# Optimization experiments

Hardware: AMD Instinct MI355X
Metric: run time of the kernel (lower is better)

## Reference

```python
import jax, jax.numpy as jnp
import numpy as np

N_SAMPLES = 4096
BACKBONE_OUT = 512
EXPANSION = 8192
NUM_CLASSES = 1000
C_COEF = 1.0


def setup_inputs() -> dict:
    key = jax.random.key(0)
    k1, k2, k3, k4 = jax.random.split(key, 4)
    X = jax.random.normal(k1, (N_SAMPLES, BACKBONE_OUT), dtype=jnp.float32)
    W_buffer = jax.random.normal(k2, (BACKBONE_OUT, EXPANSION), dtype=jnp.float32) / np.sqrt(BACKBONE_OUT)
    W_main = jax.random.normal(k3, (EXPANSION, NUM_CLASSES), dtype=jnp.float32) / np.sqrt(EXPANSION)
    W_comp = jax.random.normal(k4, (EXPANSION, NUM_CLASSES), dtype=jnp.float32) / np.sqrt(EXPANSION)
    return {"X": X, "W_buffer": W_buffer, "W_main": W_main, "W_comp": W_comp, "k": 500}


def _knn_mean_cosine(Xe, k):
    # Xe: [N, D]. Cosine kNN (excluding self), then mean of neighbor features.
    N = Xe.shape[0]
    Xn = Xe / jnp.linalg.norm(Xe, axis=1, keepdims=True)
    sim = Xn @ Xn.T                                      # [N, N]
    diag = jnp.arange(N)
    sim = sim.at[diag, diag].set(-jnp.inf)               # exclude self (== indices[:,1:])
    _, idx = jax.lax.top_k(sim, k)                       # [N, k] nearest by cosine
    # Gather-mean via binary adjacency matmul (avoids [N,k,D] intermediate).
    rows = jnp.repeat(diag, k)
    A = jnp.zeros((N, N), Xe.dtype).at[rows, idx.reshape(-1)].set(1.0)
    return (A @ Xe) / jnp.asarray(k, Xe.dtype)           # [N, D]


def reference(X, W_buffer, W_main, W_comp, k):
    Xe = X @ W_buffer                                    # random buffer expansion [N, D]
    X_main = jnp.maximum(Xe, 0.0) @ W_main               # relu -> main analytic linear
    X_knn = _knn_mean_cosine(Xe, k)
    X_comp = jnp.tanh(X_knn) @ W_comp                    # tanh -> compensation linear
    return X_main + C_COEF * X_comp
```

## Files before the change

kernel.cpp:

```cpp
#include <hip/hip_runtime.h>
#include <hip/hip_bf16.h>

#define MSAMP 4096
#define D0    512
#define EXPN  8192
#define NCLS  1000
#define NPAD  1024
#define QSCALE     (6.0f / 127.0f)
#define QSCALE_INV (127.0f / 6.0f)

typedef __attribute__((ext_vector_type(8))) _Float16       half8;
typedef __attribute__((ext_vector_type(8))) unsigned short ushort8v;
typedef __attribute__((ext_vector_type(4))) float          f32x4;
typedef __attribute__((ext_vector_type(4))) int            i32x4v;

__device__ __forceinline__ unsigned short f2h(float f) {
    union { _Float16 h; unsigned short u; } c; c.h = (_Float16)f; return c.u;
}
__device__ __forceinline__ float h2f(unsigned short u) {
    union { unsigned short u; _Float16 h; } c; c.u = u; return (float)c.h;
}
__device__ __forceinline__ ushort8v relu8h(ushort8v v) {
#pragma unroll
    for (int j = 0; j < 8; ++j) v[j] = (v[j] & 0x8000u) ? (unsigned short)0 : v[j];
    return v;
}
__device__ __forceinline__ half8 as_half8(const unsigned short* p) {
    return *(const half8*)p;
}
__device__ __forceinline__ float tanh_fast(float x) {
    float e = __expf(2.0f * x);
    return 1.0f - 2.0f * __builtin_amdgcn_rcpf(e + 1.0f);
}

__global__ __launch_bounds__(256) void cvt_x(const float* __restrict__ src,
                                             unsigned short* __restrict__ dst)
{
    const size_t i = ((size_t)blockIdx.x * 256 + threadIdx.x) * 8;
    float4 v0 = *(const float4*)(src + i), v1 = *(const float4*)(src + i + 4);
    union { unsigned short u[8]; ushort8v v; } H;
    H.u[0] = f2h(v0.x); H.u[1] = f2h(v0.y); H.u[2] = f2h(v0.z); H.u[3] = f2h(v0.w);
    H.u[4] = f2h(v1.x); H.u[5] = f2h(v1.y); H.u[6] = f2h(v1.z); H.u[7] = f2h(v1.w);
    *(ushort8v*)(dst + i) = H.v;
}

__global__ void transpose_wb(const float* __restrict__ src,
                             unsigned short* __restrict__ dst)
{
    __shared__ float t[32][33];
    const int n0 = blockIdx.x * 32, k0 = blockIdx.y * 32;
    const int tx = threadIdx.x, ty = threadIdx.y;
#pragma unroll
    for (int i = 0; i < 4; ++i)
        t[ty + 8 * i][tx] = src[(size_t)(k0 + ty + 8 * i) * EXPN + n0 + tx];
    __syncthreads();
#pragma unroll
    for (int i = 0; i < 4; ++i)
        dst[(size_t)(n0 + ty + 8 * i) * D0 + k0 + tx] = f2h(t[tx][ty + 8 * i]);
}

__global__ __launch_bounds__(256) void gemm_xe_mfma(
    const unsigned short* __restrict__ Xh, const unsigned short* __restrict__ WbT,
    unsigned short* __restrict__ Xe)
{
    __shared__ __align__(16) char smem[34816];
    unsigned short (*AsF)[64][8] = (unsigned short (*)[64][8])(smem);
    unsigned short (*BsF)[64][8] = (unsigned short (*)[64][8])(smem + 8192);

    const int tid = threadIdx.x;
    const int wid = tid >> 6, lane = tid & 63;
    const int l15 = lane & 15, q = lane >> 4;
    const int wm = (wid >> 1) * 64, wn = (wid & 1) * 64;
    const int row0 = blockIdx.y * 128, col0 = blockIdx.x * 128;

    const int sr = tid >> 1;
    const int scp = (tid & 1) * 2;
    const int mi_w = sr >> 4, l_w = sr & 15;

    f32x4 acc[4][4];
#pragma unroll
    for (int m = 0; m < 4; ++m)
#pragma unroll
        for (int n = 0; n < 4; ++n) acc[m][n] = (f32x4){0.f, 0.f, 0.f, 0.f};

    for (int k0 = 0; k0 < D0; k0 += 32) {
        const unsigned short* pa = Xh  + (size_t)(row0 + sr) * D0 + k0 + scp * 8;
        const unsigned short* pb = WbT + (size_t)(col0 + sr) * D0 + k0 + scp * 8;
        ushort8v a0 = *(const ushort8v*)pa, a1 = *(const ushort8v*)(pa + 8);
        ushort8v b0 = *(const ushort8v*)pb, b1 = *(const ushort8v*)(pb + 8);

        __syncthreads();
        *(ushort8v*)&AsF[mi_w][scp * 16 + l_w][0] = a0;
        *(ushort8v*)&AsF[mi_w][(scp + 1) * 16 + l_w][0] = a1;
        *(ushort8v*)&BsF[mi_w][scp * 16 + l_w][0] = b0;
        *(ushort8v*)&BsF[mi_w][(scp + 1) * 16 + l_w][0] = b1;
        __syncthreads();

        half8 fa[4], fb[4];
#pragma unroll
        for (int m = 0; m < 4; ++m) {
            fa[m] = as_half8(&AsF[(wm >> 4) + m][lane][0]);
            fb[m] = as_half8(&BsF[(wn >> 4) + m][lane][0]);
        }
#pragma unroll
        for (int m = 0; m < 4; ++m)
#pragma unroll
            for (int n = 0; n < 4; ++n)
                acc[m][n] = __builtin_amdgcn_mfma_f32_16x16x32_f16(fa[m], fb[n], acc[m][n], 0, 0, 0);
    }

    unsigned short (*Cb)[136] = (unsigned short (*)[136])smem;
    const int rr = tid >> 1, hh = (tid & 1) * 64;
    __syncthreads();
#pragma unroll
    for (int m = 0; m < 4; ++m)
#pragma unroll
        for (int n = 0; n < 4; ++n)
#pragma unroll
            for (int r = 0; r < 4; ++r)
                Cb[wm + m * 16 + q * 4 + r][wn + n * 16 + l15] = f2h(acc[m][n][r]);
    __syncthreads();
#pragma unroll
    for (int c = 0; c < 8; ++c)
        *(ushort8v*)&Xe[(size_t)(row0 + rr) * EXPN + col0 + hh + c * 8] =
            *(const ushort8v*)&Cb[rr][hh + c * 8];
}

__global__ __launch_bounds__(256) void gemm_sim(
    const unsigned short* __restrict__ Xe,
    const float* __restrict__ invn, float* __restrict__ Sm)
{
    __shared__ unsigned short AsF[8][64][8], BsF[8][64][8];

    const int t = blockIdx.x;
    int bj = (int)((sqrtf(8.0f * t + 1.0f) - 1.0f) * 0.5f);
    while ((bj + 1) * (bj + 2) / 2 <= t) ++bj;
    while (bj * (bj + 1) / 2 > t) --bj;
    const int bi = t - bj * (bj + 1) / 2;
    const int row0 = bi * 128, col0 = bj * 128;

    const int tid = threadIdx.x;
    const int wid = tid >> 6, lane = tid & 63;
    const int l15 = lane & 15, q = lane >> 4;
    const int wm = (wid >> 1) * 64, wn = (wid & 1) * 64;

    const int sr = tid >> 1;
    const int scp = (tid & 1) * 2;
    const int mi_w = sr >> 4, l_w = sr & 15;

    f32x4 acc[4][4];
#pragma unroll
    for (int m = 0; m < 4; ++m)
#pragma unroll
        for (int n = 0; n < 4; ++n) acc[m][n] = (f32x4){0.f, 0.f, 0.f, 0.f};

    for (int k0 = 0; k0 < EXPN; k0 += 32) {
        const unsigned short* pa = Xe + (size_t)(row0 + sr) * EXPN + k0 + scp * 8;
        const unsigned short* pb = Xe + (size_t)(col0 + sr) * EXPN + k0 + scp * 8;
        ushort8v a0 = *(const ushort8v*)pa, a1 = *(const ushort8v*)(pa + 8);
        ushort8v b0 = *(const ushort8v*)pb, b1 = *(const ushort8v*)(pb + 8);

        __syncthreads();
        *(ushort8v*)&AsF[mi_w][scp * 16 + l_w][0] = a0;
        *(ushort8v*)&AsF[mi_w][(scp + 1) * 16 + l_w][0] = a1;
        *(ushort8v*)&BsF[mi_w][scp * 16 + l_w][0] = b0;
        *(ushort8v*)&BsF[mi_w][(scp + 1) * 16 + l_w][0] = b1;
        __syncthreads();

        half8 fa[4], fb[4];
#pragma unroll
        for (int m = 0; m < 4; ++m) {
            fa[m] = as_half8(&AsF[(wm >> 4) + m][lane][0]);
            fb[m] = as_half8(&BsF[(wn >> 4) + m][lane][0]);
        }
#pragma unroll
        for (int m = 0; m < 4; ++m)
#pragma unroll
            for (int n = 0; n < 4; ++n)
                acc[m][n] = __builtin_amdgcn_mfma_f32_16x16x32_f16(fa[m], fb[n], acc[m][n], 0, 0, 0);
    }

    const bool mirror = (bi != bj);
#pragma unroll
    for (int m = 0; m < 4; ++m)
#pragma unroll
        for (int n = 0; n < 4; ++n) {
            const int gj = col0 + wn + n * 16 + l15;
            const float invj = invn[gj];
#pragma unroll
            for (int r = 0; r < 4; ++r) {
                const int gi = row0 + wm + m * 16 + q * 4 + r;
                float v = acc[m][n][r] * invn[gi] * invj;
                if (gi == gj) v = -3.0e38f;
                Sm[(size_t)gi * MSAMP + gj] = v;
                if (mirror) Sm[(size_t)gj * MSAMP + gi] = v;
            }
        }
}

__global__ __launch_bounds__(256) void gemm_adj_i8(
    const unsigned* __restrict__ Abits, const signed char* __restrict__ XeT,
    unsigned short* __restrict__ Tk, const int* __restrict__ kp)
{
    __shared__ signed char BsF[8][64][16];
    __shared__ uint2 aw2[128];

    const int tid = threadIdx.x;
    const int wid = tid >> 6, lane = tid & 63;
    const int l15 = lane & 15, q = lane >> 4;
    const int wm = (wid >> 1) * 64, wn = (wid & 1) * 64;
    const int row0 = blockIdx.x * 128;
    const int col0 = blockIdx.y * 128;

    const int sr = tid >> 1;
    const int half = tid & 1;

    i32x4v acc[4][4];
#pragma unroll
    for (int m = 0; m < 4; ++m)
#pragma unroll
        for (int n = 0; n < 4; ++n) acc[m][n] = (i32x4v){0, 0, 0, 0};

    for (int k0 = 0; k0 < MSAMP; k0 += 64) {
        const signed char* pb = XeT + (size_t)(col0 + sr) * MSAMP + k0 + half * 32;
        i32x4v b0 = *(const i32x4v*)pb;
        i32x4v b1 = *(const i32x4v*)(pb + 16);
        uint2 wv = make_uint2(0u, 0u);
        if (tid < 128)
            wv = *(const uint2*)(Abits + (size_t)(row0 + tid) * (MSAMP / 32) + (k0 >> 5));

        __syncthreads();
        *(i32x4v*)&BsF[sr >> 4][(half * 2 + 0) * 16 + (sr & 15)][0] = b0;
        *(i32x4v*)&BsF[sr >> 4][(half * 2 + 1) * 16 + (sr & 15)][0] = b1;
        if (tid < 128) aw2[tid] = wv;
        __syncthreads();

        i32x4v fb[4];
#pragma unroll
        for (int n = 0; n < 4; ++n)
            fb[n] = *(const i32x4v*)&BsF[(wn >> 4) + n][lane][0];

#pragma unroll
        for (int m = 0; m < 4; ++m) {
            const uint2 ww = aw2[wm + m * 16 + l15];
            const unsigned w = (q >= 2) ? ww.y : ww.x;
            const unsigned hw = (q & 1) ? (w >> 16) : w;
            i32x4v fa;
#pragma unroll
            for (int p = 0; p < 4; ++p)
                fa[p] = (int)((((hw >> (4 * p)) & 0xFu) * 0x00204081u) & 0x01010101u);
#pragma unroll
            for (int n = 0; n < 4; ++n)
                acc[m][n] = __builtin_amdgcn_mfma_i32_16x16x64_i8(fa, fb[n], acc[m][n], 0, 0, 0);
        }
    }

    const float kv = QSCALE / (float)(*kp);
#pragma unroll
    for (int m = 0; m < 4; ++m)
#pragma unroll
        for (int n = 0; n < 4; ++n) {
            const int gj = col0 + wn + n * 16 + l15;
#pragma unroll
            for (int r = 0; r < 4; ++r) {
                const int gi = row0 + wm + m * 16 + q * 4 + r;
                Tk[(size_t)gi * EXPN + gj] = f2h(tanh_fast((float)acc[m][n][r] * kv));
            }
        }
}

__global__ void transpose_w(const float* __restrict__ src,
                            unsigned short* __restrict__ dst)
{
    __shared__ float t[32][33];
    const int k0 = blockIdx.x * 32, n0 = blockIdx.y * 32;
    const int tx = threadIdx.x, ty = threadIdx.y;
#pragma unroll
    for (int i = 0; i < 4; ++i) {
        const int n = n0 + tx;
        t[ty + 8 * i][tx] = (n < NCLS) ? src[(size_t)(k0 + ty + 8 * i) * NCLS + n] : 0.f;
    }
    __syncthreads();
#pragma unroll
    for (int i = 0; i < 4; ++i)
        dst[(size_t)(n0 + ty + 8 * i) * EXPN + k0 + tx] = f2h(t[tx][ty + 8 * i]);
}

__global__ __launch_bounds__(256) void gemm_out_split(
    const unsigned short* __restrict__ Xe, const unsigned short* __restrict__ Tk,
    const unsigned short* __restrict__ WmT, const unsigned short* __restrict__ WcT,
    float* __restrict__ Cout, unsigned short* __restrict__ Pf)
{
    __shared__ unsigned short AsF[8][64][8], BsF[8][64][8];

    const int tid = threadIdx.x;
    const int wid = tid >> 6, lane = tid & 63;
    const int l15 = lane & 15, q = lane >> 4;
    const int wm = (wid >> 1) * 64, wn = (wid & 1) * 64;
    const int row0 = blockIdx.y * 128;
    const int col0 = blockIdx.x * 128;
    const int zz = blockIdx.z;
    const bool xe_side = (zz < 2);
    const int kbase = (zz & 1) * (EXPN / 2);

    const unsigned short* Abase = xe_side ? Xe : Tk;
    const unsigned short* Bbase = xe_side ? WmT : WcT;

    const int sr = tid >> 1;
    const int scp = (tid & 1) * 2;
    const int mi_w = sr >> 4, l_w = sr & 15;

    f32x4 acc[4][4];
#pragma unroll
    for (int m = 0; m < 4; ++m)
#pragma unroll
        for (int n = 0; n < 4; ++n) acc[m][n] = (f32x4){0.f, 0.f, 0.f, 0.f};

    for (int kk = 0; kk < EXPN / 2; kk += 32) {
        const int k0 = kbase + kk;
        const unsigned short* pa = Abase + (size_t)(row0 + sr) * EXPN + k0 + scp * 8;
        const unsigned short* pb = Bbase + (size_t)(col0 + sr) * EXPN + k0 + scp * 8;
        ushort8v a0 = *(const ushort8v*)pa, a1 = *(const ushort8v*)(pa + 8);
        ushort8v b0 = *(const ushort8v*)pb, b1 = *(const ushort8v*)(pb + 8);
        if (xe_side) { a0 = relu8h(a0); a1 = relu8h(a1); }

        __syncthreads();
        *(ushort8v*)&AsF[mi_w][scp * 16 + l_w][0] = a0;
        *(ushort8v*)&AsF[mi_w][(scp + 1) * 16 + l_w][0] = a1;
        *(ushort8v*)&BsF[mi_w][scp * 16 + l_w][0] = b0;
        *(ushort8v*)&BsF[mi_w][(scp + 1) * 16 + l_w][0] = b1;
        __syncthreads();

        half8 fa[4], fb[4];
#pragma unroll
        for (int m = 0; m < 4; ++m) {
            fa[m] = as_half8(&AsF[(wm >> 4) + m][lane][0]);
            fb[m] = as_half8(&BsF[(wn >> 4) + m][lane][0]);
        }
#pragma unroll
        for (int m = 0; m < 4; ++m)
#pragma unroll
            for (int n = 0; n < 4; ++n)
                acc[m][n] = __builtin_amdgcn_mfma_f32_16x16x32_f16(fa[m], fb[n], acc[m][n], 0, 0, 0);
    }

    if (zz == 0) {
#pragma unroll
        for (int m = 0; m < 4; ++m)
#pragma unroll
            for (int n = 0; n < 4; ++n) {
                const int gj = col0 + wn + n * 16 + l15;
                if (gj < NCLS) {
#pragma unroll
                    for (int r = 0; r < 4; ++r) {
                        const int gi = row0 + wm + m * 16 + q * 4 + r;
                        Cout[(size_t)gi * NCLS + gj] = acc[m][n][r];
                    }
                }
            }
    } else {
        unsigned short* dp = Pf + (size_t)(zz - 1) * MSAMP * NCLS;
#pragma unroll
        for (int m = 0; m < 4; ++m)
#pragma unroll
            for (int n = 0; n < 4; ++n) {
                const int gj = col0 + wn + n * 16 + l15;
                if (gj < NCLS) {
#pragma unroll
                    for (int r = 0; r < 4; ++r) {
                        const int gi = row0 + wm + m * 16 + q * 4 + r;
                        dp[(size_t)gi * NCLS + gj] = f2h(acc[m][n][r]);
                    }
                }
            }
    }
}

__global__ __launch_bounds__(256) void add_partials(float* __restrict__ out,
                                                    const unsigned short* __restrict__ P,
                                                    int n4)
{
    const int i = blockIdx.x * 256 + threadIdx.x;
    if (i < n4) {
        float4 a = ((const float4*)out)[i];
        const ushort4 p0 = *(const ushort4*)(P + (size_t)i * 4);
        const ushort4 p1 = *(const ushort4*)(P + (size_t)MSAMP * NCLS + (size_t)i * 4);
        const ushort4 p2 = *(const ushort4*)(P + (size_t)2 * MSAMP * NCLS + (size_t)i * 4);
        a.x += h2f(p0.x) + h2f(p1.x) + h2f(p2.x);
        a.y += h2f(p0.y) + h2f(p1.y) + h2f(p2.y);
        a.z += h2f(p0.z) + h2f(p1.z) + h2f(p2.z);
        a.w += h2f(p0.w) + h2f(p1.w) + h2f(p2.w);
        ((float4*)out)[i] = a;
    }
}

__global__ __launch_bounds__(256) void row_invnorm(
    const unsigned short* __restrict__ Xe, float* __restrict__ invn)
{
    const int row = blockIdx.x;
    float s = 0.f;
    for (int j = threadIdx.x * 8; j < EXPN; j += 2048) {
        ushort8v h = *(const ushort8v*)(Xe + (size_t)row * EXPN + j);
#pragma unroll
        for (int c = 0; c < 8; ++c) { float x = h2f(h[c]); s += x * x; }
    }
#pragma unroll
    for (int off = 32; off > 0; off >>= 1) s += __shfl_down(s, off);
    __shared__ float wsum[4];
    if ((threadIdx.x & 63) == 0) wsum[threadIdx.x >> 6] = s;
    __syncthreads();
    if (threadIdx.x == 0)
        invn[row] = rsqrtf(wsum[0] + wsum[1] + wsum[2] + wsum[3]);
}

__global__ __launch_bounds__(256) void topk_thresh(const float* __restrict__ sim,
                                                   float* __restrict__ thr,
                                                   int N, const int* __restrict__ kp)
{
    const int row = blockIdx.x;
    const float* srow = sim + (size_t)row * N;
    __shared__ int hist[256];
    __shared__ unsigned s_prefix;
    __shared__ int s_rem;
    if (threadIdx.x == 0) { s_prefix = 0u; s_rem = *kp; }
    __syncthreads();

    for (int pass = 0; pass < 4; ++pass) {
        const int shift = 24 - 8 * pass;
        hist[threadIdx.x] = 0;
        __syncthreads();
        const unsigned prefix = s_prefix;
        const unsigned pmask = (pass == 0) ? 0u : (0xFFFFFFFFu << (shift + 8));
        for (int j = threadIdx.x; j < N; j += 256) {
            unsigned u = __float_as_uint(srow[j]);
            u = ((int)u < 0) ? ~u : (u | 0x80000000u);
            if ((u & pmask) == (prefix & pmask))
                atomicAdd(&hist[(u >> shift) & 255], 1);
        }
        __syncthreads();
        if (threadIdx.x == 0) {
            int rem = s_rem, accum = 0, b;
            for (b = 255; b > 0; --b) {
                if (accum + hist[b] >= rem) break;
                accum += hist[b];
            }
            s_rem = rem - accum;
            s_prefix = prefix | ((unsigned)b << shift);
        }
        __syncthreads();
    }

    if (threadIdx.x == 0) {
        const unsigned u = s_prefix;
        const unsigned orig = (u & 0x80000000u) ? (u & 0x7FFFFFFFu) : ~u;
        thr[row] = __uint_as_float(orig);
    }
}

__global__ __launch_bounds__(128) void bitpack(const float* __restrict__ Sm,
                                               const float* __restrict__ thr,
                                               unsigned* __restrict__ Abits)
{
    const int row = blockIdx.x;
    const int w = threadIdx.x;
    const float t = thr[row];
    const float* p = Sm + (size_t)row * MSAMP + w * 32;
    unsigned m = 0;
#pragma unroll
    for (int b = 0; b < 32; b += 4) {
        float4 v = *(const float4*)(p + b);
        m |= (v.x >= t ? 1u : 0u) << (b + 0);
        m |= (v.y >= t ? 1u : 0u) << (b + 1);
        m |= (v.z >= t ? 1u : 0u) << (b + 2);
        m |= (v.w >= t ? 1u : 0u) << (b + 3);
    }
    Abits[(size_t)row * (MSAMP / 32) + w] = m;
}

__global__ void transpose_xe_q(const unsigned short* __restrict__ src,
                               signed char* __restrict__ dst)
{
    __shared__ signed char t[32][36];
    const int bx = blockIdx.x;
    const int by = blockIdx.y;
    const int tx = threadIdx.x, ty = threadIdx.y;
#pragma unroll
    for (int i = 0; i < 4; ++i) {
        float v = h2f(src[(size_t)(by * 32 + ty + 8 * i) * EXPN + bx * 32 + tx]);
        int qv = (int)rintf(v * QSCALE_INV);
        qv = max(-127, min(127, qv));
        t[tx][ty + 8 * i] = (signed char)qv;
    }
    __syncthreads();
    const int tid = ty * 32 + tx;
    const int nl = tid >> 3, mg = (tid & 7) * 4;
    char4 o;
    o.x = t[nl][mg + 0]; o.y = t[nl][mg + 1];
    o.z = t[nl][mg + 2]; o.w = t[nl][mg + 3];
    *(char4*)&dst[(size_t)(bx * 32 + nl) * MSAMP + by * 32 + mg] = o;
}

extern "C" void kernel_launch(void* const* d_in, const int* in_sizes, int n_in,
                              void* d_out, int out_size, void* d_ws, size_t ws_size,
                              hipStream_t stream)
{
    const float* X  = (const float*)d_in[0];
    const float* Wb = (const float*)d_in[1];
    const float* Wm = (const float*)d_in[2];
    const float* Wc = (const float*)d_in[3];
    const int*   kp = (const int*)d_in[4];
    float* out = (float*)d_out;

    char* base = (char*)d_ws;
    const size_t SEG = (size_t)64 << 20;
    const size_t need = 3 * SEG + ((size_t)2 << 20) + 65536;
    if (ws_size < need) return;

    unsigned short* Xe   = (unsigned short*)base;
    signed char*    XeTq = (signed char*)(base + SEG);
    unsigned short* WmT  = (unsigned short*)(base + SEG);
    unsigned short* WcT  = WmT + (size_t)NPAD * EXPN;
    unsigned short* Pf   = (unsigned short*)(base + SEG + ((size_t)32 << 20));
    unsigned short* Xh   = (unsigned short*)(base + 2 * SEG);
    unsigned short* WbT  = Xh + (size_t)MSAMP * D0;
    float*          Sm   = (float*)(base + 2 * SEG);
    unsigned short* Tk   = (unsigned short*)(base + 2 * SEG);
    unsigned*       Abits= (unsigned*)(base + 3 * SEG);
    float*          invn = (float*)(base + 3 * SEG + ((size_t)2 << 20));
    float*          thr  = invn + MSAMP;

    const dim3 blk(256);

    cvt_x<<<dim3((MSAMP * D0) / (256 * 8)), blk, 0, stream>>>(X, Xh);
    transpose_wb<<<dim3(EXPN / 32, D0 / 32), dim3(32, 8), 0, stream>>>(Wb, WbT);

    gemm_xe_mfma<<<dim3(EXPN / 128, MSAMP / 128), blk, 0, stream>>>(Xh, WbT, Xe);

    row_invnorm<<<dim3(MSAMP), blk, 0, stream>>>(Xe, invn);

    gemm_sim<<<dim3(528), blk, 0, stream>>>(Xe, invn, Sm);

    topk_thresh<<<dim3(MSAMP), blk, 0, stream>>>(Sm, thr, MSAMP, kp);

    bitpack<<<dim3(MSAMP), dim3(128), 0, stream>>>(Sm, thr, Abits);

    transpose_xe_q<<<dim3(EXPN / 32, MSAMP / 32), dim3(32, 8), 0, stream>>>(Xe, XeTq);

    gemm_adj_i8<<<dim3(MSAMP / 128, EXPN / 128), blk, 0, stream>>>(Abits, XeTq, Tk, kp);

    transpose_w<<<dim3(EXPN / 32, NPAD / 32), dim3(32, 8), 0, stream>>>(Wm, WmT);
    transpose_w<<<dim3(EXPN / 32, NPAD / 32), dim3(32, 8), 0, stream>>>(Wc, WcT);

    gemm_out_split<<<dim3(NPAD / 128, MSAMP / 128, 4), blk, 0, stream>>>(
        Xe, Tk, WmT, WcT, out, Pf);

    add_partials<<<dim3((MSAMP * NCLS / 4 + 255) / 256), blk, 0, stream>>>(
        out, Pf, MSAMP * NCLS / 4);
}
```

Baseline: 1.020 ms.

## Use direct global-to-LDS loads in GEMM kernels and swizzle block order

Result: slower. 1.181 ms (+15.8%).

```diff
diff --git a/kernel.cpp b/kernel.cpp
--- a/kernel.cpp
+++ b/kernel.cpp
@@ -28,9 +28,17 @@
 __device__ __forceinline__ half8 as_half8(const unsigned short* p) {
     return *(const half8*)p;
 }
+__device__ __forceinline__ half8 u2h8(ushort8v v) {
+    union { ushort8v u; half8 h; } c; c.u = v; return c.h;
+}
 __device__ __forceinline__ float tanh_fast(float x) {
     float e = __expf(2.0f * x);
     return 1.0f - 2.0f * __builtin_amdgcn_rcpf(e + 1.0f);
+}
+__device__ __forceinline__ void gl16(const void* g, void* l) {
+    __builtin_amdgcn_global_load_lds(
+        (const __attribute__((address_space(1))) unsigned int*)g,
+        (__attribute__((address_space(3))) unsigned int*)l, 16, 0, 0);
 }
 
 __global__ __launch_bounds__(256) void cvt_x(const float* __restrict__ src,
@@ -73,9 +81,10 @@
     const int wm = (wid >> 1) * 64, wn = (wid & 1) * 64;
     const int row0 = blockIdx.y * 128, col0 = blockIdx.x * 128;
 
-    const int sr = tid >> 1;
-    const int scp = (tid & 1) * 2;
-    const int mi_w = sr >> 4, l_w = sr & 15;
+    const int fr = wid * 2;
+    const int lk = q * 8;
+    const unsigned short* pa0 = Xh  + (size_t)(row0 + fr * 16 + l15) * D0 + lk;
+    const unsigned short* pb0 = WbT + (size_t)(col0 + fr * 16 + l15) * D0 + lk;
 
     f32x4 acc[4][4];
 #pragma unroll
@@ -84,16 +93,11 @@
         for (int n = 0; n < 4; ++n) acc[m][n] = (f32x4){0.f, 0.f, 0.f, 0.f};
 
     for (int k0 = 0; k0 < D0; k0 += 32) {
-        const unsigned short* pa = Xh  + (size_t)(row0 + sr) * D0 + k0 + scp * 8;
-        const unsigned short* pb = WbT + (size_t)(col0 + sr) * D0 + k0 + scp * 8;
-        ushort8v a0 = *(const ushort8v*)pa, a1 = *(const ushort8v*)(pa + 8);
-        ushort8v b0 = *(const ushort8v*)pb, b1 = *(const ushort8v*)(pb + 8);
-
-        __syncthreads();
-        *(ushort8v*)&AsF[mi_w][scp * 16 + l_w][0] = a0;
-        *(ushort8v*)&AsF[mi_w][(scp + 1) * 16 + l_w][0] = a1;
-        *(ushort8v*)&BsF[mi_w][scp * 16 + l_w][0] = b0;
-        *(ushort8v*)&BsF[mi_w][(scp + 1) * 16 + l_w][0] = b1;
+        __syncthreads();
+        gl16(pa0 + k0,            &AsF[fr][0][0]);
+        gl16(pa0 + 16 * D0 + k0,  &AsF[fr + 1][0][0]);
+        gl16(pb0 + k0,            &BsF[fr][0][0]);
+        gl16(pb0 + 16 * D0 + k0,  &BsF[fr + 1][0][0]);
         __syncthreads();
 
         half8 fa[4], fb[4];
@@ -132,7 +136,8 @@
 {
     __shared__ unsigned short AsF[8][64][8], BsF[8][64][8];
 
-    const int t = blockIdx.x;
+    int t = blockIdx.x;
+    t = (t & 7) * 66 + (t >> 3);
     int bj = (int)((sqrtf(8.0f * t + 1.0f) - 1.0f) * 0.5f);
     while ((bj + 1) * (bj + 2) / 2 <= t) ++bj;
     while (bj * (bj + 1) / 2 > t) --bj;
@@ -144,9 +149,10 @@
     const int l15 = lane & 15, q = lane >> 4;
     const int wm = (wid >> 1) * 64, wn = (wid & 1) * 64;
 
-    const int sr = tid >> 1;
-    const int scp = (tid & 1) * 2;
-    const int mi_w = sr >> 4, l_w = sr & 15;
+    const int fr = wid * 2;
+    const int lk = q * 8;
+    const unsigned short* pa0 = Xe + (size_t)(row0 + fr * 16 + l15) * EXPN + lk;
+    const unsigned short* pb0 = Xe + (size_t)(col0 + fr * 16 + l15) * EXPN + lk;
 
     f32x4 acc[4][4];
 #pragma unroll
@@ -155,16 +161,11 @@
         for (int n = 0; n < 4; ++n) acc[m][n] = (f32x4){0.f, 0.f, 0.f, 0.f};
 
     for (int k0 = 0; k0 < EXPN; k0 += 32) {
-        const unsigned short* pa = Xe + (size_t)(row0 + sr) * EXPN + k0 + scp * 8;
-        const unsigned short* pb = Xe + (size_t)(col0 + sr) * EXPN + k0 + scp * 8;
-        ushort8v a0 = *(const ushort8v*)pa, a1 = *(const ushort8v*)(pa + 8);
-        ushort8v b0 = *(const ushort8v*)pb, b1 = *(const ushort8v*)(pb + 8);
-
-        __syncthreads();
-        *(ushort8v*)&AsF[mi_w][scp * 16 + l_w][0] = a0;
-        *(ushort8v*)&AsF[mi_w][(scp + 1) * 16 + l_w][0] = a1;
-        *(ushort8v*)&BsF[mi_w][scp * 16 + l_w][0] = b0;
-        *(ushort8v*)&BsF[mi_w][(scp + 1) * 16 + l_w][0] = b1;
+        __syncthreads();
+        gl16(pa0 + k0,              &AsF[fr][0][0]);
+        gl16(pa0 + 16 * EXPN + k0,  &AsF[fr + 1][0][0]);
+        gl16(pb0 + k0,              &BsF[fr][0][0]);
+        gl16(pb0 + 16 * EXPN + k0,  &BsF[fr + 1][0][0]);
         __syncthreads();
 
         half8 fa[4], fb[4];
@@ -209,11 +210,14 @@
     const int wid = tid >> 6, lane = tid & 63;
     const int l15 = lane & 15, q = lane >> 4;
     const int wm = (wid >> 1) * 64, wn = (wid & 1) * 64;
-    const int row0 = blockIdx.x * 128;
-    const int col0 = blockIdx.y * 128;
-
-    const int sr = tid >> 1;
-    const int half = tid & 1;
+
+    int lin = blockIdx.x + blockIdx.y * 32;
+    lin = (lin & 7) * 256 + (lin >> 3);
+    const int row0 = (lin & 31) * 128;
+    const int col0 = (lin >> 5) * 128;
+
+    const int fr = wid * 2;
+    const signed char* pb0 = XeT + (size_t)(col0 + fr * 16 + l15) * MSAMP + q * 16;
 
     i32x4v acc[4][4];
 #pragma unroll
@@ -222,16 +226,13 @@
         for (int n = 0; n < 4; ++n) acc[m][n] = (i32x4v){0, 0, 0, 0};
 
     for (int k0 = 0; k0 < MSAMP; k0 += 64) {
-        const signed char* pb = XeT + (size_t)(col0 + sr) * MSAMP + k0 + half * 32;
-        i32x4v b0 = *(const i32x4v*)pb;
-        i32x4v b1 = *(const i32x4v*)(pb + 16);
         uint2 wv = make_uint2(0u, 0u);
         if (tid < 128)
             wv = *(const uint2*)(Abits + (size_t)(row0 + tid) * (MSAMP / 32) + (k0 >> 5));
 
         __syncthreads();
-        *(i32x4v*)&BsF[sr >> 4][(half * 2 + 0) * 16 + (sr & 15)][0] = b0;
-        *(i32x4v*)&BsF[sr >> 4][(half * 2 + 1) * 16 + (sr & 15)][0] = b1;
+        gl16(pb0 + k0,               &BsF[fr][0][0]);
+        gl16(pb0 + 16 * MSAMP + k0,  &BsF[fr + 1][0][0]);
         if (tid < 128) aw2[tid] = wv;
         __syncthreads();
 
@@ -297,18 +298,22 @@
     const int wid = tid >> 6, lane = tid & 63;
     const int l15 = lane & 15, q = lane >> 4;
     const int wm = (wid >> 1) * 64, wn = (wid & 1) * 64;
-    const int row0 = blockIdx.y * 128;
-    const int col0 = blockIdx.x * 128;
-    const int zz = blockIdx.z;
+
+    int lin = blockIdx.x + blockIdx.y * 8 + blockIdx.z * 256;
+    lin = (lin & 7) * 128 + (lin >> 3);
+    const int col0 = (lin & 7) * 128;
+    const int row0 = ((lin >> 3) & 31) * 128;
+    const int zz = lin >> 8;
     const bool xe_side = (zz < 2);
     const int kbase = (zz & 1) * (EXPN / 2);
 
     const unsigned short* Abase = xe_side ? Xe : Tk;
     const unsigned short* Bbase = xe_side ? WmT : WcT;
 
-    const int sr = tid >> 1;
-    const int scp = (tid & 1) * 2;
-    const int mi_w = sr >> 4, l_w = sr & 15;
+    const int fr = wid * 2;
+    const int lk = q * 8;
+    const unsigned short* pa0 = Abase + (size_t)(row0 + fr * 16 + l15) * EXPN + kbase + lk;
+    const unsigned short* pb0 = Bbase + (size_t)(col0 + fr * 16 + l15) * EXPN + kbase + lk;
 
     f32x4 acc[4][4];
 #pragma unroll
@@ -317,24 +322,19 @@
         for (int n = 0; n < 4; ++n) acc[m][n] = (f32x4){0.f, 0.f, 0.f, 0.f};
 
     for (int kk = 0; kk < EXPN / 2; kk += 32) {
-        const int k0 = kbase + kk;
-        const unsigned short* pa = Abase + (size_t)(row0 + sr) * EXPN + k0 + scp * 8;
-        const unsigned short* pb = Bbase + (size_t)(col0 + sr) * EXPN + k0 + scp * 8;
-        ushort8v a0 = *(const ushort8v*)pa, a1 = *(const ushort8v*)(pa + 8);
-        ushort8v b0 = *(const ushort8v*)pb, b1 = *(const ushort8v*)(pb + 8);
-        if (xe_side) { a0 = relu8h(a0); a1 = relu8h(a1); }
-
-        __syncthreads();
-        *(ushort8v*)&AsF[mi_w][scp * 16 + l_w][0] = a0;
-        *(ushort8v*)&AsF[mi_w][(scp + 1) * 16 + l_w][0] = a1;
-        *(ushort8v*)&BsF[mi_w][scp * 16 + l_w][0] = b0;
-        *(ushort8v*)&BsF[mi_w][(scp + 1) * 16 + l_w][0] = b1;
+        __syncthreads();
+        gl16(pa0 + kk,              &AsF[fr][0][0]);
+        gl16(pa0 + 16 * EXPN + kk,  &AsF[fr + 1][0][0]);
+        gl16(pb0 + kk,              &BsF[fr][0][0]);
+        gl16(pb0 + 16 * EXPN + kk,  &BsF[fr + 1][0][0]);
         __syncthreads();
 
         half8 fa[4], fb[4];
 #pragma unroll
         for (int m = 0; m < 4; ++m) {
-            fa[m] = as_half8(&AsF[(wm >> 4) + m][lane][0]);
+            ushort8v ua = *(const ushort8v*)&AsF[(wm >> 4) + m][lane][0];
+            if (xe_side) ua = relu8h(ua);
+            fa[m] = u2h8(ua);
             fb[m] = as_half8(&BsF[(wn >> 4) + m][lane][0]);
         }
 #pragma unroll
```
